# Kernel tuning notes

Measured on AMD Instinct MI355X. Metric: run time of the kernel, lower is better.

## Reference

```python
import jax, jax.numpy as jnp
import numpy as np

B, N, C = 8, 4096, 1024
ATT_DIM = 512
M = 64  # num_outputs


def setup_inputs() -> dict:
    key = jax.random.key(0)
    k_x, k_w, k_b, k_av = jax.random.split(key, 4)
    x = jax.random.normal(k_x, (B, N, C), dtype=jnp.float32)
    # nn.Linear(input_dim, attention_dim): weight (att, C), bias (att,)
    lim = 1.0 / np.sqrt(C)
    W = jax.random.uniform(k_w, (ATT_DIM, C), dtype=jnp.float32, minval=-lim, maxval=lim)
    b = jax.random.uniform(k_b, (ATT_DIM,), dtype=jnp.float32, minval=-lim, maxval=lim)
    # torch.rand -> uniform [0,1)
    attention_vectors = jax.random.uniform(k_av, (M, ATT_DIM), dtype=jnp.float32)
    return {"x": x, "W": W, "b": b, "attention_vectors": attention_vectors}


def reference(x, W, b, attention_vectors):
    # linear projection: (B,N,C) @ (C,att) + bias -> (B,N,att)
    scores = jnp.einsum('bnc,dc->bnd', x, W) + b
    # learned-query attention logits: (B,M,N)
    logits = jnp.einsum('bnd,md->bmn', scores, attention_vectors)
    weights = jax.nn.softmax(logits, axis=-1)
    # pool original features: (B,M,N) @ (B,N,C) -> (B,M,C)
    return jnp.einsum('bmn,bnc->bmc', weights, x)
```

## Files before the change

kernel.cpp:

```cpp
#include <hip/hip_runtime.h>
#include <hip/hip_bf16.h>

#define Bn 8
#define Nn 4096
#define Cn 1024
#define Dn 512
#define Mn 64

typedef __hip_bfloat16 bf16;
typedef __attribute__((ext_vector_type(8))) short short8;
typedef __attribute__((ext_vector_type(4))) short short4x;
typedef __attribute__((ext_vector_type(4))) float f32x4;

#define MFMA16(a, b, c) __builtin_amdgcn_mfma_f32_16x16x32_bf16((a), (b), (c), 0, 0, 0)

__device__ inline short bfbits(float f) {
  union { bf16 b; short s; } u;
  u.b = __float2bfloat16(f);
  return u.s;
}

__global__ __launch_bounds__(256) void prep_kernel(
    const float* __restrict__ W, const float* __restrict__ bias,
    const float* __restrict__ av, bf16* __restrict__ Vhi,
    bf16* __restrict__ Vlo, float* __restrict__ c0) {
  const int m = blockIdx.x;
  const int t = threadIdx.x;
  const int cl = t & 63, dg = t >> 6;
  const int c = blockIdx.y * 64 + cl;
  const float* wp = W + (size_t)(dg * 128) * Cn + c;
  const float* ap = av + m * Dn + dg * 128;
  float a0 = 0.f, a1 = 0.f, a2 = 0.f, a3 = 0.f;
#pragma unroll 8
  for (int i = 0; i < 128; i += 4) {
    a0 = fmaf(ap[i + 0], wp[(size_t)(i + 0) * Cn], a0);
    a1 = fmaf(ap[i + 1], wp[(size_t)(i + 1) * Cn], a1);
    a2 = fmaf(ap[i + 2], wp[(size_t)(i + 2) * Cn], a2);
    a3 = fmaf(ap[i + 3], wp[(size_t)(i + 3) * Cn], a3);
  }
  __shared__ float red[256];
  red[t] = (a0 + a1) + (a2 + a3);
  __syncthreads();
  const float v = red[cl] + red[cl + 64] + red[cl + 128] + red[cl + 192];
  if (dg == 0) {
    const bf16 hi = __float2bfloat16(v);
    Vhi[m * Cn + c] = hi;
    Vlo[m * Cn + c] = __float2bfloat16(v - __bfloat162float(hi));
  }
  if (blockIdx.y == 0) {
    __syncthreads();
    red[t] = av[m * Dn + t] * bias[t] + av[m * Dn + t + 256] * bias[t + 256];
    __syncthreads();
    if (t < 64) {
      float s = red[t] + red[t + 64] + red[t + 128] + red[t + 192];
#pragma unroll
      for (int off = 32; off > 0; off >>= 1) s += __shfl_down(s, off);
      if (t == 0) c0[m] = s;
    }
  }
}

__global__ __launch_bounds__(256) void logits_kernel(
    const float* __restrict__ x, const bf16* __restrict__ Vhi,
    const bf16* __restrict__ Vlo, const float* __restrict__ c0,
    float* __restrict__ logits) {
  const int n0 = blockIdx.x * 64;
  const int b = blockIdx.y;
  const int t = threadIdx.x;
  __shared__ short Xs[64][136];
  __shared__ short VsH[64][136];
  __shared__ short VsL[64][136];
  const int w = t >> 6, lane = t & 63, lr = lane & 15, q = lane >> 4;
  const ptrdiff_t dlo = Vlo - Vhi;

  int ur[4], uc[4];
  const float* xsrc[4];
  const bf16* hsrc[4];
#pragma unroll
  for (int j = 0; j < 4; ++j) {
    const int u = t + 256 * j;
    ur[j] = u >> 4;
    uc[j] = (u & 15) * 8;
    xsrc[j] = x + (size_t)(b * Nn + n0 + ur[j]) * Cn + uc[j];
    hsrc[j] = Vhi + ur[j] * Cn + uc[j];
  }

  f32x4 acc[4];
#pragma unroll
  for (int i = 0; i < 4; ++i) acc[i] = (f32x4){0.f, 0.f, 0.f, 0.f};

  float4 px0[4], px1[4];
  short8 pvh[4], pvl[4];
#pragma unroll
  for (int j = 0; j < 4; ++j) {
    px0[j] = *(const float4*)(xsrc[j]);
    px1[j] = *(const float4*)(xsrc[j] + 4);
    pvh[j] = *(const short8*)(hsrc[j]);
    pvl[j] = *(const short8*)(hsrc[j] + dlo);
  }

  for (int k0 = 0; k0 < Cn; k0 += 128) {
#pragma unroll
    for (int j = 0; j < 4; ++j) {
      short8 s;
      s[0] = bfbits(px0[j].x); s[1] = bfbits(px0[j].y);
      s[2] = bfbits(px0[j].z); s[3] = bfbits(px0[j].w);
      s[4] = bfbits(px1[j].x); s[5] = bfbits(px1[j].y);
      s[6] = bfbits(px1[j].z); s[7] = bfbits(px1[j].w);
      *(short8*)&Xs[ur[j]][uc[j]] = s;
      *(short8*)&VsH[ur[j]][uc[j]] = pvh[j];
      *(short8*)&VsL[ur[j]][uc[j]] = pvl[j];
    }
    __syncthreads();
    if (k0 + 128 < Cn) {
#pragma unroll
      for (int j = 0; j < 4; ++j) {
        px0[j] = *(const float4*)(xsrc[j] + k0 + 128);
        px1[j] = *(const float4*)(xsrc[j] + k0 + 132);
        pvh[j] = *(const short8*)(hsrc[j] + k0 + 128);
        pvl[j] = *(const short8*)(hsrc[j] + dlo + k0 + 128);
      }
    }
#pragma unroll
    for (int kk = 0; kk < 128; kk += 32) {
      const short8 a = *(const short8*)&Xs[w * 16 + lr][kk + q * 8];
#pragma unroll
      for (int mt = 0; mt < 4; ++mt) {
        acc[mt] = MFMA16(a, *(const short8*)&VsH[mt * 16 + lr][kk + q * 8], acc[mt]);
        acc[mt] = MFMA16(a, *(const short8*)&VsL[mt * 16 + lr][kk + q * 8], acc[mt]);
      }
    }
    __syncthreads();
  }
#pragma unroll
  for (int mt = 0; mt < 4; ++mt) {
    const int m = mt * 16 + lr;
    const float bb = c0[m];
    float4 o;
    o.x = acc[mt][0] + bb; o.y = acc[mt][1] + bb;
    o.z = acc[mt][2] + bb; o.w = acc[mt][3] + bb;
    *(float4*)&logits[(size_t)(b * Mn + m) * Nn + n0 + w * 16 + q * 4] = o;
  }
}

__global__ __launch_bounds__(256) void softmax_kernel(
    const float* __restrict__ logits, bf16* __restrict__ wgt) {
  const int row = blockIdx.x;
  const int t = threadIdx.x;
  const float* L = logits + (size_t)row * Nn;
  float v[16];
  float mx = -3.4e38f;
#pragma unroll
  for (int i = 0; i < 16; ++i) {
    v[i] = L[t + 256 * i];
    mx = fmaxf(mx, v[i]);
  }
#pragma unroll
  for (int off = 32; off > 0; off >>= 1) mx = fmaxf(mx, __shfl_down(mx, off));
  __shared__ float sred[4];
  if ((t & 63) == 0) sred[t >> 6] = mx;
  __syncthreads();
  mx = fmaxf(fmaxf(sred[0], sred[1]), fmaxf(sred[2], sred[3]));
  float sum = 0.f;
#pragma unroll
  for (int i = 0; i < 16; ++i) {
    v[i] = __expf(v[i] - mx);
    sum += v[i];
  }
#pragma unroll
  for (int off = 32; off > 0; off >>= 1) sum += __shfl_down(sum, off);
  __syncthreads();
  if ((t & 63) == 0) sred[t >> 6] = sum;
  __syncthreads();
  const float inv = 1.f / (sred[0] + sred[1] + sred[2] + sred[3]);
#pragma unroll
  for (int i = 0; i < 16; ++i)
    wgt[(size_t)row * Nn + t + 256 * i] = __float2bfloat16(v[i] * inv);
}

__global__ __launch_bounds__(256) void pool_kernel(
    const float* __restrict__ x, const bf16* __restrict__ wgt,
    float* __restrict__ part) {
  const int cbase = blockIdx.x * 64;
  const int b = blockIdx.y;
  const int ks = blockIdx.z;
  const int t = threadIdx.x;
  __shared__ short XT[64][136];
  const int w = t >> 6, lane = t & 63, lr = lane & 15, q = lane >> 4;
  const int mh = (w & 1) * 32, ch = (w >> 1) * 32;
  f32x4 acc[2][2];
#pragma unroll
  for (int i = 0; i < 2; ++i)
#pragma unroll
    for (int j = 0; j < 2; ++j) acc[i][j] = (f32x4){0.f, 0.f, 0.f, 0.f};

  const int h = t & 15, g = t >> 4;
  const int swz = 8 * (h & 7);
  const int swzr0 = 8 * (((ch + lr) >> 2) & 7);
  const int swzr1 = 8 * (((ch + 16 + lr) >> 2) & 7);
  const int kbase = ks * (Nn / 4);
  const float* xsrc = x + (size_t)b * Nn * Cn + (size_t)(kbase + 4 * g) * Cn + cbase + 4 * h;
  const bf16* wr0 = wgt + (size_t)(b * Mn + mh + lr) * Nn + kbase;
  const bf16* wr1 = wr0 + (size_t)16 * Nn;

  float4 pf[8];
#pragma unroll
  for (int i = 0; i < 4; ++i) {
    pf[i]     = *(const float4*)(xsrc + (size_t)i * Cn);
    pf[4 + i] = *(const float4*)(xsrc + (size_t)(64 + i) * Cn);
  }

  for (int kc = 0; kc < Nn / 4; kc += 128) {
#pragma unroll
    for (int blk = 0; blk < 2; ++blk) {
      const float4 r0 = pf[blk * 4 + 0], r1 = pf[blk * 4 + 1];
      const float4 r2 = pf[blk * 4 + 2], r3 = pf[blk * 4 + 3];
      const int kof = (blk * 64 + 4 * g) ^ swz;
      short4x v0, v1, v2, v3;
      v0[0] = bfbits(r0.x); v0[1] = bfbits(r1.x); v0[2] = bfbits(r2.x); v0[3] = bfbits(r3.x);
      v1[0] = bfbits(r0.y); v1[1] = bfbits(r1.y); v1[2] = bfbits(r2.y); v1[3] = bfbits(r3.y);
      v2[0] = bfbits(r0.z); v2[1] = bfbits(r1.z); v2[2] = bfbits(r2.z); v2[3] = bfbits(r3.z);
      v3[0] = bfbits(r0.w); v3[1] = bfbits(r1.w); v3[2] = bfbits(r2.w); v3[3] = bfbits(r3.w);
      *(short4x*)&XT[4 * h + 0][kof] = v0;
      *(short4x*)&XT[4 * h + 1][kof] = v1;
      *(short4x*)&XT[4 * h + 2][kof] = v2;
      *(short4x*)&XT[4 * h + 3][kof] = v3;
    }
    __syncthreads();
    if (kc + 128 < Nn / 4) {
#pragma unroll
      for (int i = 0; i < 4; ++i) {
        pf[i]     = *(const float4*)(xsrc + (size_t)(kc + 128 + i) * Cn);
        pf[4 + i] = *(const float4*)(xsrc + (size_t)(kc + 192 + i) * Cn);
      }
    }
#pragma unroll
    for (int kk = 0; kk < 128; kk += 32) {
      const short8 a0 = *(const short8*)(wr0 + kc + kk + q * 8);
      const short8 a1 = *(const short8*)(wr1 + kc + kk + q * 8);
      const short8 b0 = *(const short8*)&XT[ch + lr][(kk + q * 8) ^ swzr0];
      const short8 b1 = *(const short8*)&XT[ch + 16 + lr][(kk + q * 8) ^ swzr1];
      acc[0][0] = MFMA16(a0, b0, acc[0][0]);
      acc[0][1] = MFMA16(a0, b1, acc[0][1]);
      acc[1][0] = MFMA16(a1, b0, acc[1][0]);
      acc[1][1] = MFMA16(a1, b1, acc[1][1]);
    }
    __syncthreads();
  }
  float* pout = part + ((size_t)ks * Bn + b) * Mn * Cn;
#pragma unroll
  for (int mi = 0; mi < 2; ++mi)
#pragma unroll
    for (int ci = 0; ci < 2; ++ci) {
      const int m = mh + mi * 16 + q * 4;
      const int c = cbase + ch + ci * 16 + lr;
#pragma unroll
      for (int reg = 0; reg < 4; ++reg)
        pout[(size_t)(m + reg) * Cn + c] = acc[mi][ci][reg];
    }
}

__global__ __launch_bounds__(256) void reduce_kernel(
    const float* __restrict__ part, float* __restrict__ out) {
  const int i = blockIdx.x * 256 + threadIdx.x;
  const float4* p = (const float4*)part;
  const int S4 = (Bn * Mn * Cn) / 4;
  const float4 v0 = p[i], v1 = p[i + S4], v2 = p[i + 2 * S4], v3 = p[i + 3 * S4];
  float4 o;
  o.x = (v0.x + v1.x) + (v2.x + v3.x);
  o.y = (v0.y + v1.y) + (v2.y + v3.y);
  o.z = (v0.z + v1.z) + (v2.z + v3.z);
  o.w = (v0.w + v1.w) + (v2.w + v3.w);
  ((float4*)out)[i] = o;
}

extern "C" void kernel_launch(void* const* d_in, const int* in_sizes, int n_in,
                              void* d_out, int out_size, void* d_ws, size_t ws_size,
                              hipStream_t stream) {
  const float* x = (const float*)d_in[0];
  const float* W = (const float*)d_in[1];
  const float* bias = (const float*)d_in[2];
  const float* av = (const float*)d_in[3];
  float* out = (float*)d_out;
  char* ws = (char*)d_ws;

  bf16* Vhi = (bf16*)(ws + 0);
  bf16* Vlo = (bf16*)(ws + 131072);
  float* c0 = (float*)(ws + 262144);
  float* logits = (float*)(ws + 263168);
  bf16* wgt = (bf16*)(ws + 8651776);
  float* part = (float*)(ws + 12846080);

  prep_kernel<<<dim3(Mn, Cn / 64), 256, 0, stream>>>(W, bias, av, Vhi, Vlo, c0);
  logits_kernel<<<dim3(Nn / 64, Bn), 256, 0, stream>>>(x, Vhi, Vlo, c0, logits);
  softmax_kernel<<<Bn * Mn, 256, 0, stream>>>(logits, wgt);
  pool_kernel<<<dim3(Cn / 64, Bn, 4), 256, 0, stream>>>(x, wgt, part);
  reduce_kernel<<<(Bn * Mn * Cn) / 1024, 256, 0, stream>>>(part, out);
}
```

Baseline: 244.4 us.

## Replace split-K partial buffer and reduce kernel with atomic accumulation, split-K 8

The pooling GEMM now splits the sequence dimension eight ways instead of four, doubling the grid to 1024 blocks. Each block atomically adds its tile into the zeroed output, so the partial-sum buffer and the separate reduce kernel go away. A small zero kernel clears the output first. This cuts partial-result traffic and one launch and raises occupancy, in exchange for float atomics, whose summation order is nondeterministic, and shorter per-block K loops.

Result: no change. 247.2 us (+1.2%).

```diff
diff --git a/kernel.cpp b/kernel.cpp
--- a/kernel.cpp
+++ b/kernel.cpp
@@ -18,6 +18,11 @@
   union { bf16 b; short s; } u;
   u.b = __float2bfloat16(f);
   return u.s;
+}
+
+__global__ __launch_bounds__(256) void zero_kernel(float* __restrict__ out) {
+  const int i = blockIdx.x * 256 + threadIdx.x;
+  ((float4*)out)[i] = (float4){0.f, 0.f, 0.f, 0.f};
 }
 
 __global__ __launch_bounds__(256) void prep_kernel(
@@ -180,7 +185,7 @@
 
 __global__ __launch_bounds__(256) void pool_kernel(
     const float* __restrict__ x, const bf16* __restrict__ wgt,
-    float* __restrict__ part) {
+    float* __restrict__ out) {
   const int cbase = blockIdx.x * 64;
   const int b = blockIdx.y;
   const int ks = blockIdx.z;
@@ -198,7 +203,8 @@
   const int swz = 8 * (h & 7);
   const int swzr0 = 8 * (((ch + lr) >> 2) & 7);
   const int swzr1 = 8 * (((ch + 16 + lr) >> 2) & 7);
-  const int kbase = ks * (Nn / 4);
+  const int NQ = Nn / 8;
+  const int kbase = ks * NQ;
   const float* xsrc = x + (size_t)b * Nn * Cn + (size_t)(kbase + 4 * g) * Cn + cbase + 4 * h;
   const bf16* wr0 = wgt + (size_t)(b * Mn + mh + lr) * Nn + kbase;
   const bf16* wr1 = wr0 + (size_t)16 * Nn;
@@ -210,7 +216,7 @@
     pf[4 + i] = *(const float4*)(xsrc + (size_t)(64 + i) * Cn);
   }
 
-  for (int kc = 0; kc < Nn / 4; kc += 128) {
+  for (int kc = 0; kc < NQ; kc += 128) {
 #pragma unroll
     for (int blk = 0; blk < 2; ++blk) {
       const float4 r0 = pf[blk * 4 + 0], r1 = pf[blk * 4 + 1];
@@ -227,7 +233,7 @@
       *(short4x*)&XT[4 * h + 3][kof] = v3;
     }
     __syncthreads();
-    if (kc + 128 < Nn / 4) {
+    if (kc + 128 < NQ) {
 #pragma unroll
       for (int i = 0; i < 4; ++i) {
         pf[i]     = *(const float4*)(xsrc + (size_t)(kc + 128 + i) * Cn);
@@ -247,7 +253,7 @@
     }
     __syncthreads();
   }
-  float* pout = part + ((size_t)ks * Bn + b) * Mn * Cn;
+  float* pout = out + (size_t)b * Mn * Cn;
 #pragma unroll
   for (int mi = 0; mi < 2; ++mi)
 #pragma unroll
@@ -256,22 +262,8 @@
       const int c = cbase + ch + ci * 16 + lr;
 #pragma unroll
       for (int reg = 0; reg < 4; ++reg)
-        pout[(size_t)(m + reg) * Cn + c] = acc[mi][ci][reg];
-    }
-}
-
-__global__ __launch_bounds__(256) void reduce_kernel(
-    const float* __restrict__ part, float* __restrict__ out) {
-  const int i = blockIdx.x * 256 + threadIdx.x;
-  const float4* p = (const float4*)part;
-  const int S4 = (Bn * Mn * Cn) / 4;
-  const float4 v0 = p[i], v1 = p[i + S4], v2 = p[i + 2 * S4], v3 = p[i + 3 * S4];
-  float4 o;
-  o.x = (v0.x + v1.x) + (v2.x + v3.x);
-  o.y = (v0.y + v1.y) + (v2.y + v3.y);
-  o.z = (v0.z + v1.z) + (v2.z + v3.z);
-  o.w = (v0.w + v1.w) + (v2.w + v3.w);
-  ((float4*)out)[i] = o;
+        atomicAdd(&pout[(size_t)(m + reg) * Cn + c], acc[mi][ci][reg]);
+    }
 }
 
 extern "C" void kernel_launch(void* const* d_in, const int* in_sizes, int n_in,
@@ -289,11 +281,10 @@
   float* c0 = (float*)(ws + 262144);
   float* logits = (float*)(ws + 263168);
   bf16* wgt = (bf16*)(ws + 8651776);
-  float* part = (float*)(ws + 12846080);
-
+
+  zero_kernel<<<(Bn * Mn * Cn) / 1024, 256, 0, stream>>>(out);
   prep_kernel<<<dim3(Mn, Cn / 64), 256, 0, stream>>>(W, bias, av, Vhi, Vlo, c0);
   logits_kernel<<<dim3(Nn / 64, Bn), 256, 0, stream>>>(x, Vhi, Vlo, c0, logits);
   softmax_kernel<<<Bn * Mn, 256, 0, stream>>>(logits, wgt);
-  pool_kernel<<<dim3(Cn / 64, Bn, 4), 256, 0, stream>>>(x, wgt, part);
-  reduce_kernel<<<(Bn * Mn * Cn) / 1024, 256, 0, stream>>>(part, out);
-}
+  pool_kernel<<<dim3(Cn / 64, Bn, 8), 256, 0, stream>>>(x, wgt, out);
+}
```

## Fuse softmax into logits kernel using per-tile online max/sum rescaling in pool

Applied to the files above, without the earlier changes.

Removes the separate softmax kernel and the fp32 logits buffer. The logits kernel now computes per-64-column tile maxima and exp-sums and writes unnormalized bf16 weights. The pool kernel combines the tile statistics into a global max and sum, then rescales each 64-wide accumulation group with a per-tile factor. This saves a full round trip of the logits through memory and one kernel launch. In exchange it adds FMA rescaling work and extra registers inside the pool inner loop.

Result: slower. 261.6 us (+7.0%).

```diff
diff --git a/kernel.cpp b/kernel.cpp
--- a/kernel.cpp
+++ b/kernel.cpp
@@ -60,11 +60,12 @@
   }
 }
 
-__global__ __launch_bounds__(256) void logits_kernel(
+__global__ __launch_bounds__(256) void logits_sm_kernel(
     const float* __restrict__ x, const bf16* __restrict__ Vhi,
     const bf16* __restrict__ Vlo, const float* __restrict__ c0,
-    float* __restrict__ logits) {
-  const int n0 = blockIdx.x * 64;
+    bf16* __restrict__ wgt, float* __restrict__ Mp, float* __restrict__ Sp) {
+  const int g = blockIdx.x;
+  const int n0 = g * 64;
   const int b = blockIdx.y;
   const int t = threadIdx.x;
   __shared__ short Xs[64][136];
@@ -132,73 +133,109 @@
     }
     __syncthreads();
   }
+
+  float* wredM = (float*)&Xs[0][0];
+  float* wredS = wredM + 256;
+  float rmax[4];
+#pragma unroll
+  for (int mt = 0; mt < 4; ++mt) {
+    float r = fmaxf(fmaxf(acc[mt][0], acc[mt][1]), fmaxf(acc[mt][2], acc[mt][3]));
+    r = fmaxf(r, __shfl_xor(r, 16));
+    r = fmaxf(r, __shfl_xor(r, 32));
+    rmax[mt] = r;
+  }
+  if (q == 0)
+#pragma unroll
+    for (int mt = 0; mt < 4; ++mt) wredM[w * 64 + mt * 16 + lr] = rmax[mt];
+  __syncthreads();
+  float vv[4][4];
 #pragma unroll
   for (int mt = 0; mt < 4; ++mt) {
     const int m = mt * 16 + lr;
-    const float bb = c0[m];
-    float4 o;
-    o.x = acc[mt][0] + bb; o.y = acc[mt][1] + bb;
-    o.z = acc[mt][2] + bb; o.w = acc[mt][3] + bb;
-    *(float4*)&logits[(size_t)(b * Mn + m) * Nn + n0 + w * 16 + q * 4] = o;
-  }
-}
-
-__global__ __launch_bounds__(256) void softmax_kernel(
-    const float* __restrict__ logits, bf16* __restrict__ wgt) {
-  const int row = blockIdx.x;
-  const int t = threadIdx.x;
-  const float* L = logits + (size_t)row * Nn;
-  float v[16];
-  float mx = -3.4e38f;
-#pragma unroll
-  for (int i = 0; i < 16; ++i) {
-    v[i] = L[t + 256 * i];
-    mx = fmaxf(mx, v[i]);
-  }
-#pragma unroll
-  for (int off = 32; off > 0; off >>= 1) mx = fmaxf(mx, __shfl_down(mx, off));
-  __shared__ float sred[4];
-  if ((t & 63) == 0) sred[t >> 6] = mx;
+    const float mp = fmaxf(fmaxf(wredM[m], wredM[64 + m]),
+                           fmaxf(wredM[128 + m], wredM[192 + m]));
+    float s = 0.f;
+#pragma unroll
+    for (int r = 0; r < 4; ++r) {
+      vv[mt][r] = __expf(acc[mt][r] - mp);
+      s += vv[mt][r];
+    }
+    s += __shfl_xor(s, 16);
+    s += __shfl_xor(s, 32);
+    if (q == 0) wredS[w * 64 + m] = s;
+  }
+#pragma unroll
+  for (int mt = 0; mt < 4; ++mt) {
+    const int m = mt * 16 + lr;
+    short4x o;
+    o[0] = bfbits(vv[mt][0]); o[1] = bfbits(vv[mt][1]);
+    o[2] = bfbits(vv[mt][2]); o[3] = bfbits(vv[mt][3]);
+    *(short4x*)&wgt[(size_t)(b * Mn + m) * Nn + n0 + w * 16 + q * 4] = o;
+  }
   __syncthreads();
-  mx = fmaxf(fmaxf(sred[0], sred[1]), fmaxf(sred[2], sred[3]));
-  float sum = 0.f;
-#pragma unroll
-  for (int i = 0; i < 16; ++i) {
-    v[i] = __expf(v[i] - mx);
-    sum += v[i];
-  }
-#pragma unroll
-  for (int off = 32; off > 0; off >>= 1) sum += __shfl_down(sum, off);
-  __syncthreads();
-  if ((t & 63) == 0) sred[t >> 6] = sum;
-  __syncthreads();
-  const float inv = 1.f / (sred[0] + sred[1] + sred[2] + sred[3]);
-#pragma unroll
-  for (int i = 0; i < 16; ++i)
-    wgt[(size_t)row * Nn + t + 256 * i] = __float2bfloat16(v[i] * inv);
+  if (w == 0) {
+    const int m = lane;
+    const float mp = fmaxf(fmaxf(wredM[m], wredM[64 + m]),
+                           fmaxf(wredM[128 + m], wredM[192 + m]));
+    const float sp = wredS[m] + wredS[64 + m] + wredS[128 + m] + wredS[192 + m];
+    Mp[((size_t)b * Mn + m) * 64 + g] = mp + c0[m];
+    Sp[((size_t)b * Mn + m) * 64 + g] = sp;
+  }
 }
 
 __global__ __launch_bounds__(256) void pool_kernel(
     const float* __restrict__ x, const bf16* __restrict__ wgt,
+    const float* __restrict__ Mp, const float* __restrict__ Sp,
     float* __restrict__ part) {
   const int cbase = blockIdx.x * 64;
   const int b = blockIdx.y;
   const int ks = blockIdx.z;
   const int t = threadIdx.x;
   __shared__ short XT[64][136];
+  __shared__ float scs[16][64];
   const int w = t >> 6, lane = t & 63, lr = lane & 15, q = lane >> 4;
   const int mh = (w & 1) * 32, ch = (w >> 1) * 32;
-  f32x4 acc[2][2];
+
+  {
+    const int m = t >> 2, qq = t & 3;
+    const float* mpp = Mp + ((size_t)b * Mn + m) * 64 + qq * 16;
+    const float* spp = Sp + ((size_t)b * Mn + m) * 64 + qq * 16;
+    float mpl[16], spl[16];
+#pragma unroll
+    for (int j = 0; j < 16; ++j) { mpl[j] = mpp[j]; spl[j] = spp[j]; }
+    float lmax = -3.4e38f;
+#pragma unroll
+    for (int j = 0; j < 16; ++j) lmax = fmaxf(lmax, mpl[j]);
+    float gmax = fmaxf(lmax, __shfl_xor(lmax, 1));
+    gmax = fmaxf(gmax, __shfl_xor(gmax, 2));
+    float lsum = 0.f;
+#pragma unroll
+    for (int j = 0; j < 16; ++j) lsum += __expf(mpl[j] - gmax) * spl[j];
+    float gsum = lsum + __shfl_xor(lsum, 1);
+    gsum = gsum + __shfl_xor(gsum, 2);
+    if (qq == ks) {
+      const float inv = 1.f / gsum;
+#pragma unroll
+      for (int j = 0; j < 16; ++j) scs[j][m] = __expf(mpl[j] - gmax) * inv;
+    }
+  }
+  __syncthreads();
+
+  f32x4 accT[2][2], accg[2][2];
 #pragma unroll
   for (int i = 0; i < 2; ++i)
 #pragma unroll
-    for (int j = 0; j < 2; ++j) acc[i][j] = (f32x4){0.f, 0.f, 0.f, 0.f};
+    for (int j = 0; j < 2; ++j) {
+      accT[i][j] = (f32x4){0.f, 0.f, 0.f, 0.f};
+      accg[i][j] = (f32x4){0.f, 0.f, 0.f, 0.f};
+    }
 
   const int h = t & 15, g = t >> 4;
   const int swz = 8 * (h & 7);
   const int swzr0 = 8 * (((ch + lr) >> 2) & 7);
   const int swzr1 = 8 * (((ch + 16 + lr) >> 2) & 7);
-  const int kbase = ks * (Nn / 4);
+  const int NQ = Nn / 4;
+  const int kbase = ks * NQ;
   const float* xsrc = x + (size_t)b * Nn * Cn + (size_t)(kbase + 4 * g) * Cn + cbase + 4 * h;
   const bf16* wr0 = wgt + (size_t)(b * Mn + mh + lr) * Nn + kbase;
   const bf16* wr1 = wr0 + (size_t)16 * Nn;
@@ -210,7 +247,7 @@
     pf[4 + i] = *(const float4*)(xsrc + (size_t)(64 + i) * Cn);
   }
 
-  for (int kc = 0; kc < Nn / 4; kc += 128) {
+  for (int kc = 0; kc < NQ; kc += 128) {
 #pragma unroll
     for (int blk = 0; blk < 2; ++blk) {
       const float4 r0 = pf[blk * 4 + 0], r1 = pf[blk * 4 + 1];
@@ -227,7 +264,7 @@
       *(short4x*)&XT[4 * h + 3][kof] = v3;
     }
     __syncthreads();
-    if (kc + 128 < Nn / 4) {
+    if (kc + 128 < NQ) {
 #pragma unroll
       for (int i = 0; i < 4; ++i) {
         pf[i]     = *(const float4*)(xsrc + (size_t)(kc + 128 + i) * Cn);
@@ -240,10 +277,23 @@
       const short8 a1 = *(const short8*)(wr1 + kc + kk + q * 8);
       const short8 b0 = *(const short8*)&XT[ch + lr][(kk + q * 8) ^ swzr0];
       const short8 b1 = *(const short8*)&XT[ch + 16 + lr][(kk + q * 8) ^ swzr1];
-      acc[0][0] = MFMA16(a0, b0, acc[0][0]);
-      acc[0][1] = MFMA16(a0, b1, acc[0][1]);
-      acc[1][0] = MFMA16(a1, b0, acc[1][0]);
-      acc[1][1] = MFMA16(a1, b1, acc[1][1]);
+      accg[0][0] = MFMA16(a0, b0, accg[0][0]);
+      accg[0][1] = MFMA16(a0, b1, accg[0][1]);
+      accg[1][0] = MFMA16(a1, b0, accg[1][0]);
+      accg[1][1] = MFMA16(a1, b1, accg[1][1]);
+      if (kk == 32 || kk == 96) {
+        const int gl = (kc + kk) >> 6;
+#pragma unroll
+        for (int mi = 0; mi < 2; ++mi)
+#pragma unroll
+          for (int r = 0; r < 4; ++r) {
+            const float s = scs[gl][mh + mi * 16 + q * 4 + r];
+            accT[mi][0][r] = fmaf(s, accg[mi][0][r], accT[mi][0][r]);
+            accT[mi][1][r] = fmaf(s, accg[mi][1][r], accT[mi][1][r]);
+            accg[mi][0][r] = 0.f;
+            accg[mi][1][r] = 0.f;
+          }
+      }
     }
     __syncthreads();
   }
@@ -256,7 +306,7 @@
       const int c = cbase + ch + ci * 16 + lr;
 #pragma unroll
       for (int reg = 0; reg < 4; ++reg)
-        pout[(size_t)(m + reg) * Cn + c] = acc[mi][ci][reg];
+        pout[(size_t)(m + reg) * Cn + c] = accT[mi][ci][reg];
     }
 }
 
@@ -287,13 +337,13 @@
   bf16* Vhi = (bf16*)(ws + 0);
   bf16* Vlo = (bf16*)(ws + 131072);
   float* c0 = (float*)(ws + 262144);
-  float* logits = (float*)(ws + 263168);
-  bf16* wgt = (bf16*)(ws + 8651776);
-  float* part = (float*)(ws + 12846080);
+  bf16* wgt = (bf16*)(ws + 263168);
+  float* Mp = (float*)(ws + 4457472);
+  float* Sp = (float*)(ws + 4588544);
+  float* part = (float*)(ws + 4719616);
 
   prep_kernel<<<dim3(Mn, Cn / 64), 256, 0, stream>>>(W, bias, av, Vhi, Vlo, c0);
-  logits_kernel<<<dim3(Nn / 64, Bn), 256, 0, stream>>>(x, Vhi, Vlo, c0, logits);
-  softmax_kernel<<<Bn * Mn, 256, 0, stream>>>(logits, wgt);
-  pool_kernel<<<dim3(Cn / 64, Bn, 4), 256, 0, stream>>>(x, wgt, part);
+  logits_sm_kernel<<<dim3(Nn / 64, Bn), 256, 0, stream>>>(x, Vhi, Vlo, c0, wgt, Mp, Sp);
+  pool_kernel<<<dim3(Cn / 64, Bn, 4), 256, 0, stream>>>(x, wgt, Mp, Sp, part);
   reduce_kernel<<<(Bn * Mn * Cn) / 1024, 256, 0, stream>>>(part, out);
 }
```
